# Kernel tuning notes

Measured on AMD Instinct MI355X. Metric: run time of the kernel, lower is better.

## Reference

```python
import jax, jax.numpy as jnp
import numpy as np

K = 5            # kernel_size per dim
KD = K ** 3      # 125 spline weight slots
DIM = 3
NUM_GRAPHS = 64
# (n_nodes, n_edges, c_in, c_mid, c_out) per pyramid level
LEVELS = [(20000, 320000, 1, 32, 64), (10000, 160000, 1, 64, 64),
          (5000, 80000, 1, 64, 64), (2500, 40000, 1, 64, 64), (1250, 20000, 1, 64, 64)]


def setup_inputs() -> dict:
    key = jax.random.key(0)
    inp = {}
    for i, (n, e, cin, c1, c2) in enumerate(LEVELS, start=1):
        ks = jax.random.split(jax.random.fold_in(key, i), 8)
        inp[f'x{i}'] = jax.random.normal(ks[0], (n, cin), jnp.float32)
        inp[f'pseudo{i}'] = jax.random.uniform(ks[1], (e, DIM), jnp.float32)  # in [0,1)
        inp[f'edge_index{i}'] = jax.random.randint(ks[2], (2, e), 0, n)
        inp[f'batch{i}'] = jnp.sort(jax.random.randint(ks[3], (n,), 0, NUM_GRAPHS))
        inp[f'W{i}a'] = 0.1 * jax.random.normal(ks[4], (KD, cin, c1), jnp.float32)
        inp[f'root{i}a'] = 0.1 * jax.random.normal(ks[5], (cin, c1), jnp.float32)
        inp[f'bias{i}a'] = jnp.zeros((c1,), jnp.float32)
        inp[f'W{i}b'] = 0.1 * jax.random.normal(ks[6], (KD, c1, c2), jnp.float32)
        inp[f'root{i}b'] = 0.1 * jax.random.normal(ks[7], (c1, c2), jnp.float32)
        inp[f'bias{i}b'] = jnp.zeros((c2,), jnp.float32)
    kf = jax.random.fold_in(key, 99)
    inp['fc_w'] = 0.05 * jax.random.normal(kf, (5 * 64, 10), jnp.float32)
    inp['fc_b'] = jnp.zeros((10,), jnp.float32)
    return inp


def _spline_conv(x, src, dst, pseudo, W, Wroot, bias):
    """Degree-1 open B-spline conv (torch_spline_conv), mean aggregation + root weight."""
    n, cin = x.shape
    v = pseudo * (K - 1)                       # [E,3], pseudo in [0,1)
    k0 = jnp.floor(v).astype(jnp.int32)        # lower knot index per dim
    frac = v - k0                              # fractional part per dim
    xs = x[src]                                # [E,cin] gather source feats
    # accumulate basis-weighted source features per (target node, kernel slot)
    acc = jnp.zeros((n, KD, cin), x.dtype)
    for bits in range(2 ** DIM):               # 8 corner combinations of linear spline
        w = jnp.ones((src.shape[0],), x.dtype)
        idx = jnp.zeros((src.shape[0],), jnp.int32)
        for d in range(DIM):
            b = (bits >> d) & 1
            w = w * (frac[:, d] if b else 1.0 - frac[:, d])
            idx = idx * K + (k0[:, d] + b)
        acc = acc.at[dst, idx].add(w[:, None] * xs)
    deg = jnp.zeros((n,), x.dtype).at[dst].add(1.0)
    out = jnp.einsum('nki,kio->no', acc, W) / jnp.maximum(deg, 1.0)[:, None]
    return out + x @ Wroot + bias


def _readout(f, batch):
    s = jax.ops.segment_sum(f, batch, num_segments=NUM_GRAPHS)
    cnt = jax.ops.segment_sum(jnp.ones((f.shape[0],), f.dtype), batch, num_segments=NUM_GRAPHS)
    return s / jnp.maximum(cnt, 1.0)[:, None]   # scatter_mean


def _level(x, ei, ps, bt, Wa, ra, ba, Wb, rb, bb):
    f = jax.nn.relu(_spline_conv(x, ei[0], ei[1], ps, Wa, ra, ba))
    f = jax.nn.relu(_spline_conv(f, ei[0], ei[1], ps, Wb, rb, bb))
    return _readout(f, bt)


def reference(x1, pseudo1, edge_index1, batch1, W1a, root1a, bias1a, W1b, root1b, bias1b,
              x2, pseudo2, edge_index2, batch2, W2a, root2a, bias2a, W2b, root2b, bias2b,
              x3, pseudo3, edge_index3, batch3, W3a, root3a, bias3a, W3b, root3b, bias3b,
              x4, pseudo4, edge_index4, batch4, W4a, root4a, bias4a, W4b, root4b, bias4b,
              x5, pseudo5, edge_index5, batch5, W5a, root5a, bias5a, W5b, root5b, bias5b,
              fc_w, fc_b):
    levels = [
        (x1, edge_index1, pseudo1, batch1, W1a, root1a, bias1a, W1b, root1b, bias1b),
        (x2, edge_index2, pseudo2, batch2, W2a, root2a, bias2a, W2b, root2b, bias2b),
        (x3, edge_index3, pseudo3, batch3, W3a, root3a, bias3a, W3b, root3b, bias3b),
        (x4, edge_index4, pseudo4, batch4, W4a, root4a, bias4a, W4b, root4b, bias4b),
        (x5, edge_index5, pseudo5, batch5, W5a, root5a, bias5a, W5b, root5b, bias5b),
    ]
    res = [_level(*lv) for lv in levels]
    h = jnp.concatenate(res, axis=1)            # [B,320]; eval mode -> dropout is identity
    logits = h @ fc_w + fc_b                    # [B,10]
    return jax.nn.log_softmax(logits, axis=1)
```

## Files before the change

### kernel.cpp

```cpp
#include <hip/hip_runtime.h>
#include <hip/hip_fp16.h>
#include <math.h>

#define NUM_GRAPHS 64

typedef unsigned short ushortT;
typedef __attribute__((ext_vector_type(8))) short bf16x8;
typedef __attribute__((ext_vector_type(4))) float f32x4;

constexpr int cN[5]       = {20000, 10000, 5000, 2500, 1250};
constexpr int cE[5]       = {320000, 160000, 80000, 40000, 20000};
constexpr int cNOFF[6]    = {0, 20000, 30000, 35000, 37500, 38750};
constexpr int cEOFF[6]    = {0, 320000, 480000, 560000, 600000, 620000};
constexpr int cEBLKOFF[6] = {0, 1250, 1875, 2188, 2345, 2424};
constexpr int cNBLKOFF[6] = {0, 79, 119, 139, 149, 154};
constexpr int cMT[5]      = {5064, 2564, 1314, 689, 377};
constexpr int cTILEOFF[6] = {0, 5064, 7628, 8942, 9631, 10008};
constexpr int cSEOFF[6]   = {0, 324096, 488192, 572288, 616384, 640512};
constexpr int cF1OFF[6]   = {0, 640000, 1280000, 1600000, 1760000, 1840000};
constexpr int cWOFF[6]    = {0, 32000, 96000, 160000, 224000, 288000};
constexpr int cABLK32[6]  = {0, 625, 938, 1095, 1174, 1214};
constexpr int cRBOFF[5]   = {0, 256, 768, 1280, 1792};
constexpr int cWAOFF[6]   = {0, 512, 1536, 2560, 3584, 4608};
constexpr int cRGB[6]     = {0, 313, 470, 549, 589, 609};
constexpr int cPAIR[6]    = {0, 2532, 3814, 4471, 4816, 5005};

struct P5f { const float* p[5]; };
struct P5i { const int* p[5]; };

__device__ __forceinline__ int lvl_e(int b) {
    return (b >= cEBLKOFF[4]) ? 4 : (b >= cEBLKOFF[3]) ? 3 : (b >= cEBLKOFF[2]) ? 2 : (b >= cEBLKOFF[1]) ? 1 : 0;
}
__device__ __forceinline__ int lvl_n(int b) {
    return (b >= cNBLKOFF[4]) ? 4 : (b >= cNBLKOFF[3]) ? 3 : (b >= cNBLKOFF[2]) ? 2 : (b >= cNBLKOFF[1]) ? 1 : 0;
}

__device__ __forceinline__ ushortT f2bf(float f) {
    union { float f; unsigned int u; } v; v.f = f;
    unsigned int r = (v.u + 0x7FFFu + ((v.u >> 16) & 1u)) >> 16;
    return (ushortT)r;
}
__device__ __forceinline__ float h2f_lo(unsigned int u) {
    return __half2float(__ushort_as_half((ushortT)(u & 0xFFFFu)));
}
__device__ __forceinline__ float h2f_hi(unsigned int u) {
    return __half2float(__ushort_as_half((ushortT)(u >> 16)));
}

__global__ void k_hist(P5f PS, P5i EI, int* __restrict__ dcnt, int* __restrict__ bb) {
    int b = blockIdx.x;
    int l = lvl_e(b);
    int lb = b - cEBLKOFF[l];
    int E = cE[l];
    __shared__ int h[64];
    int t = threadIdx.x;
    if (t < 64) h[t] = 0;
    __syncthreads();
    int e = lb * 256 + t;
    if (e < E) {
        atomicAdd(&dcnt[cNOFF[l] + EI.p[l][E + e]], 1);
        const float* ps = PS.p[l];
        int c = (int)floorf(ps[e * 3] * 4.f) * 16 + (int)floorf(ps[e * 3 + 1] * 4.f) * 4
              + (int)floorf(ps[e * 3 + 2] * 4.f);
        atomicAdd(&h[c], 1);
    }
    __syncthreads();
    if (t < 64) bb[(size_t)b * 64 + t] = h[t];
}

__global__ void k_cellscan(int* __restrict__ bb_all, int* __restrict__ csPad,
                           int* __restrict__ cellTot, int* __restrict__ cot_all) {
    int l = blockIdx.x;
    int c = threadIdx.x;
    int* bb = bb_all + (size_t)cEBLKOFF[l] * 64;
    int nblk = cEBLKOFF[l + 1] - cEBLKOFF[l];
    int run = 0;
    int b = 0;
    for (; b + 16 <= nblk; b += 16) {
        int v[16];
#pragma unroll
        for (int u = 0; u < 16; u++) v[u] = bb[(b + u) * 64 + c];
#pragma unroll
        for (int u = 0; u < 16; u++) { bb[(b + u) * 64 + c] = run; run += v[u]; }
    }
    for (; b < nblk; b++) { int v = bb[b * 64 + c]; bb[b * 64 + c] = run; run += v; }
    int tot = run;
    cellTot[l * 64 + c] = tot;
    int tiles = (tot + 63) >> 6;
    int x = tiles;
#pragma unroll
    for (int off = 1; off < 64; off <<= 1) { int y = __shfl_up(x, off, 64); if (c >= off) x += y; }
    int tileBase = x - tiles;
    csPad[l * 64 + c] = tileBase * 64;
    int* cot = cot_all + cTILEOFF[l];
    for (int i = 0; i < tiles; i++) {
        int vv = tot - (i << 6); if (vv > 64) vv = 64;
        cot[tileBase + i] = c | (vv << 8);
    }
    int nT = __shfl(x, 63, 64);
    int mt = cMT[l];
    for (int i = nT + c; i < mt; i += 64) cot[i] = -1;
}

__global__ void k_nscan1(const int* __restrict__ dcnt, int* __restrict__ dbase, int* __restrict__ bsum) {
    int b = blockIdx.x;
    int l = lvl_n(b);
    int lb = b - cNBLKOFF[l];
    int n = cN[l];
    __shared__ int sh[256];
    int t = threadIdx.x;
    int i = lb * 256 + t;
    int v = (i < n) ? dcnt[cNOFF[l] + i] : 0;
    sh[t] = v;
    __syncthreads();
    for (int off = 1; off < 256; off <<= 1) {
        int y = (t >= off) ? sh[t - off] : 0;
        __syncthreads();
        sh[t] += y;
        __syncthreads();
    }
    if (i < n) dbase[cNOFF[l] + i] = sh[t] - v;
    if (t == 255) bsum[b] = sh[255];
}

__global__ void k_nscan2(const int* __restrict__ bsum, int* __restrict__ boff) {
    int l = blockIdx.x;
    int o = cNBLKOFF[l];
    int nb = cNBLKOFF[l + 1] - o;
    int t = threadIdx.x;
    int v = (t < nb) ? bsum[o + t] : 0;
    int s = v;
#pragma unroll
    for (int off = 1; off < 64; off <<= 1) { int y = __shfl_up(s, off, 64); if (t >= off) s += y; }
    int tot = __shfl(s, 63, 64);
    if (t < nb) boff[o + t] = s - v;
    int t2 = t + 64;
    int v2 = (t2 < nb) ? bsum[o + t2] : 0;
    int s2 = v2;
#pragma unroll
    for (int off = 1; off < 64; off <<= 1) { int y = __shfl_up(s2, off, 64); if (t >= off) s2 += y; }
    if (t2 < nb) boff[o + t2] = tot + s2 - v2;
}

__global__ void k_scatter(P5f PS, P5i EI, const int* __restrict__ bb, const int* __restrict__ csPad,
                          const int* __restrict__ dbase, const int* __restrict__ boff,
                          int* __restrict__ rank,
                          int4* __restrict__ cbrec, int4* __restrict__ darec,
                          int* __restrict__ cpos) {
    int b = blockIdx.x;
    int l = lvl_e(b);
    int lb = b - cEBLKOFF[l];
    int E = cE[l];
    __shared__ int base[64];
    __shared__ int cnt[64];
    int t = threadIdx.x;
    if (t < 64) { base[t] = bb[(size_t)b * 64 + t] + csPad[l * 64 + t]; cnt[t] = 0; }
    __syncthreads();
    int e = lb * 256 + t;
    if (e >= E) return;
    const float* ps = PS.p[l];
    float v0 = ps[e * 3] * 4.f, v1 = ps[e * 3 + 1] * 4.f, v2 = ps[e * 3 + 2] * 4.f;
    float f0 = floorf(v0), f1v = floorf(v1), f2v = floorf(v2);
    int c = (int)f0 * 16 + (int)f1v * 4 + (int)f2v;
    int r = atomicAdd(&cnt[c], 1);
    int posc = base[c] + r;
    const int* ei = EI.p[l];
    int src = ei[e];
    int dst = ei[E + e];
    int posd = dbase[cNOFF[l] + dst] + boff[cNBLKOFF[l] + (dst >> 8)]
             + atomicAdd(&rank[cNOFF[l] + dst], 1);
    unsigned int fxfy = (unsigned int)__half_as_ushort(__float2half(v0 - f0))
                      | ((unsigned int)__half_as_ushort(__float2half(v1 - f1v)) << 16);
    unsigned int fzp  = (unsigned int)__half_as_ushort(__float2half(v2 - f2v));
    int4 rc;
    rc.x = src; rc.y = 0; rc.z = (int)fxfy; rc.w = (int)fzp;
    cbrec[cSEOFF[l] + posc] = rc;
    int4 rd;
    rd.x = src | (dst << 16); rd.y = c; rd.z = (int)fxfy; rd.w = (int)fzp;
    darec[cEOFF[l] + posd] = rd;
    cpos[cEOFF[l] + posd] = posc;
}

__global__ void k_wswz(P5f WB, P5f RootB, P5f WA,
                       uint4* __restrict__ hi4, uint4* __restrict__ rb, uint4* __restrict__ wa) {
    int idx = blockIdx.x * 256 + threadIdx.x;
    if (idx >= 294912) return;
    if (idx < 288000) {
        int l = (idx >= 224000) ? 4 : (idx >= 160000) ? 3 : (idx >= 96000) ? 2 : (idx >= 32000) ? 1 : 0;
        int local = idx - cWOFF[l];
        int T = l ? 2 : 1, C = l ? 64 : 32;
        int lane = local & 63;
        int blk = (local >> 6) & 3;
        int rest = local >> 8;
        int st = rest % T, s = rest / T;
        int q = lane >> 4, n = blk * 16 + (lane & 15);
        const float* W = WB.p[l];
        union { ushortT u[8]; uint4 v; } ph;
#pragma unroll
        for (int j = 0; j < 8; j++) {
            int k = st * 32 + q * 8 + j;
            ph.u[j] = f2bf(W[((size_t)s * C + k) * 64 + n]);
        }
        hi4[idx] = ph.v;
    } else if (idx < 290304) {
        int id2 = idx - 288000;
        int l = (id2 >= 1792) ? 4 : (id2 >= 1280) ? 3 : (id2 >= 768) ? 2 : (id2 >= 256) ? 1 : 0;
        int local = id2 - cRBOFF[l];
        int lane = local & 63;
        int w = (local >> 6) & 3;
        int st = local >> 8;
        int q = lane >> 4, n = w * 16 + (lane & 15);
        const float* R = RootB.p[l];
        union { ushortT u[8]; uint4 v; } ph;
#pragma unroll
        for (int j = 0; j < 8; j++) {
            int k = st * 32 + q * 8 + j;
            ph.u[j] = f2bf(R[k * 64 + n]);
        }
        rb[id2] = ph.v;
    } else {
        int id3 = idx - 290304;
        int l = (id3 >= cWAOFF[4]) ? 4 : (id3 >= cWAOFF[3]) ? 3 : (id3 >= cWAOFF[2]) ? 2 : (id3 >= cWAOFF[1]) ? 1 : 0;
        int local = id3 - cWAOFF[l];
        int C1 = l ? 64 : 32;
        int numN = C1 / 16;
        int lane = local & 63;
        int rest = local >> 6;
        int nb = rest % numN, st = rest / numN;
        int q = lane >> 4, n = nb * 16 + (lane & 15);
        const float* Wsrc = WA.p[l];
        union { ushortT u[8]; uint4 v; } ph;
#pragma unroll
        for (int j = 0; j < 8; j++) {
            int k = st * 32 + q * 8 + j;
            ph.u[j] = (k < 125) ? f2bf(Wsrc[k * C1 + n]) : (ushortT)0;
        }
        wa[id3] = ph.v;
    }
}

__launch_bounds__(256)
__global__ void conv_a_fused(P5f X, P5f RootA, P5f BiasA,
                             const int4* __restrict__ darec, const uint4* __restrict__ wasw,
                             const int* __restrict__ dbase, const int* __restrict__ boff,
                             const int* __restrict__ dcnt, ushortT* __restrict__ f1bf) {
    __shared__ float S[32 * 126];
    __shared__ int infoS[256];
    __shared__ unsigned int fxyS[256];
    __shared__ unsigned int fzS[256];
    __shared__ float xsS[256];
    int b = blockIdx.x;
    int l = (b >= cABLK32[4]) ? 4 : (b >= cABLK32[3]) ? 3 : (b >= cABLK32[2]) ? 2 : (b >= cABLK32[1]) ? 1 : 0;
    int node0 = (b - cABLK32[l]) * 32;
    int n = cN[l];
    int nn = n - node0; if (nn > 32) nn = 32;
    int t = threadIdx.x;
    int lane = t & 63, wv = t >> 6;
    int C1 = l ? 64 : 32;
    int numN = C1 >> 4;
    int nTask = 2 * numN;
    const uint4* wl = wasw + cWAOFF[l];
    uint4 wfrag0[4], wfrag1[4];
    {
        int w0 = wv % numN;
#pragma unroll
        for (int st = 0; st < 4; st++) wfrag0[st] = wl[(st * numN + w0) * 64 + lane];
        if (nTask == 8) {
            int w1 = wv;
#pragma unroll
            for (int st = 0; st < 4; st++) wfrag1[st] = wl[(st * numN + w1) * 64 + lane];
        }
    }
    for (int i = t; i < 32 * 126; i += 256) S[i] = 0.f;
    const int* db = dbase + cNOFF[l];
    const int* bo = boff + cNBLKOFF[l];
    int estart = db[node0] + bo[node0 >> 8];
    int vend = node0 + nn;
    int eend = (vend >= n) ? cE[l] : (db[vend] + bo[vend >> 8]);
    const float* x = X.p[l];
    const int4* dr = darec + cEOFF[l];
    const int bx = t & 1, by = (t >> 1) & 1, bz = (t >> 2) & 1;
    int4 rcur; float xcur;
    if (estart + t < eend) { rcur = dr[estart + t]; xcur = x[rcur.x & 0xFFFF]; }
    for (int cs = estart; cs < eend; cs += 256) {
        if (cs + t < eend) {
            infoS[t] = ((((unsigned int)rcur.x) >> 16) - node0) * 64 + rcur.y;
            fxyS[t] = (unsigned int)rcur.z;
            fzS[t] = (unsigned int)rcur.w;
            xsS[t] = xcur;
        }
        __syncthreads();
        int pn = cs + 256 + t;
        if (pn < eend) { rcur = dr[pn]; xcur = x[rcur.x & 0xFFFF]; }
        int ne = eend - cs; if (ne > 256) ne = 256;
        for (int j = (t >> 3); j < ne; j += 32) {
            int info = infoS[j];
            int nl = info >> 6, cell = info & 63;
            unsigned int uz = fxyS[j];
            float fx = h2f_lo(uz), fy = h2f_hi(uz), fz = h2f_lo(fzS[j]);
            float xs = xsS[j];
            int cx = cell >> 4, cy = (cell >> 2) & 3, cz = cell & 3;
            int slot = (cx + bx) * 25 + (cy + by) * 5 + (cz + bz);
            float wc = (bx ? fx : 1.f - fx) * (by ? fy : 1.f - fy) * (bz ? fz : 1.f - fz);
            atomicAdd(&S[nl * 126 + slot], wc * xs);
        }
        __syncthreads();
    }
    ushortT* Sbf = (ushortT*)S;
    float v[17];
#pragma unroll
    for (int j = 0; j < 17; j++) {
        int i = t + 256 * j;
        int node = i / 136, k = i % 136;
        v[j] = (i < 4352 && k < 126) ? S[node * 126 + k] : 0.f;
    }
    __syncthreads();
#pragma unroll
    for (int j = 0; j < 17; j++) {
        int i = t + 256 * j;
        if (i < 4352) Sbf[i] = f2bf(v[j]);
    }
    __syncthreads();
    int q = lane >> 4, m = lane & 15;
    const int* dcl = dcnt + cNOFF[l];
    ushortT* f1bfl = f1bf + cF1OFF[l];
    auto do_task = [&](int task, const uint4* wf) {
        int g = task / numN;
        int w = task - g * numN;
        f32x4 acc = (f32x4){0.f, 0.f, 0.f, 0.f};
#pragma unroll
        for (int st = 0; st < 4; st++) {
            bf16x8 a = *(const bf16x8*)&Sbf[(16 * g + m) * 136 + st * 32 + q * 8];
            bf16x8 bw = __builtin_bit_cast(bf16x8, wf[st]);
            acc = __builtin_amdgcn_mfma_f32_16x16x32_bf16(a, bw, acc, 0, 0, 0);
        }
        int ch = w * 16 + m;
        float rv = RootA.p[l][ch], bv = BiasA.p[l][ch];
#pragma unroll
        for (int rr = 0; rr < 4; rr++) {
            int row = 16 * g + q * 4 + rr;
            if (row < nn) {
                int gnode = node0 + row;
                int dv = dcl[gnode];
                float d = (float)(dv > 1 ? dv : 1);
                float o = acc[rr] / d + x[gnode] * rv + bv;
                f1bfl[(size_t)gnode * C1 + ch] = f2bf(fmaxf(o, 0.f));
            }
        }
    };
    do_task(wv, wfrag0);
    if (nTask == 8) do_task(wv + 4, wfrag1);
}

__launch_bounds__(256)
__global__ void k_rgemm(const ushortT* __restrict__ f1bf, const uint4* __restrict__ rb,
                        float* __restrict__ f2) {
    int b = blockIdx.x;
    int l = (b >= cRGB[4]) ? 4 : (b >= cRGB[3]) ? 3 : (b >= cRGB[2]) ? 2 : (b >= cRGB[1]) ? 1 : 0;
    int node0 = (b - cRGB[l]) * 64;
    int n = cN[l];
    int nn = n - node0; if (nn > 64) nn = 64;
    int t = threadIdx.x;
    int lane = t & 63, w = t >> 6;
    int q = lane >> 4, m = lane & 15;
    const int CIN = l ? 64 : 32;
    const int T = l ? 2 : 1;
    const ushortT* fl = f1bf + cF1OFF[l];
    const uint4* rbl = rb + cRBOFF[l];
    f32x4 C[4];
#pragma unroll
    for (int mt = 0; mt < 4; mt++) C[mt] = (f32x4){0.f, 0.f, 0.f, 0.f};
    for (int st = 0; st < T; st++) {
        bf16x8 bh = __builtin_bit_cast(bf16x8, rbl[(st * 4 + w) * 64 + lane]);
#pragma unroll
        for (int mt = 0; mt < 4; mt++) {
            int row = 16 * mt + m;
            int nr = node0 + row; if (nr > n - 1) nr = n - 1;
            bf16x8 a = *(const bf16x8*)&fl[(size_t)nr * CIN + st * 32 + q * 8];
            C[mt] = __builtin_amdgcn_mfma_f32_16x16x32_bf16(a, bh, C[mt], 0, 0, 0);
        }
    }
#pragma unroll
    for (int mt = 0; mt < 4; mt++)
#pragma unroll
        for (int rr = 0; rr < 4; rr++) {
            int row = 16 * mt + q * 4 + rr;
            if (row < nn)
                f2[(size_t)(cNOFF[l] + node0 + row) * 64 + 16 * w + m] = C[mt][rr];
        }
}

template<int CIN>
__device__ __forceinline__ void stage_issue(const ushortT* __restrict__ f1bfl, int srcx,
                                            ushortT* lregion, int lane) {
    const int NC = CIN / 8;
#pragma unroll
    for (int i = 0; i < NC; i++) {
        int s = i * 64 + lane;
        int row = s / NC;
        int cp = s & (NC - 1);
        int chunk = cp ^ (row & (NC - 1));
        int src = __shfl(srcx, row, 64);
        const ushortT* gp = f1bfl + (size_t)src * CIN + chunk * 8;
        __builtin_amdgcn_global_load_lds(
            (const __attribute__((address_space(1))) void*)gp,
            (__attribute__((address_space(3))) void*)(lregion + (size_t)i * 512),
            16, 0, 0);
    }
}

template<int CIN>
__device__ __forceinline__ void read_ahr(const ushortT* st, bf16x8 (&ahr)[4][CIN / 32],
                                         int q, int m) {
    const int NC = CIN / 8;
#pragma unroll
    for (int mt = 0; mt < 4; mt++) {
        int row = 16 * mt + m;
#pragma unroll
        for (int s = 0; s < CIN / 32; s++) {
            int chunk = s * 4 + q;
            int cp = chunk ^ (row & (NC - 1));
            ahr[mt][s] = *(const bf16x8*)&st[(size_t)row * NC * 8 + cp * 8];
        }
    }
}

template<int CIN>
__device__ __forceinline__ void conv_b_tile_compute(
    const uint4* __restrict__ whiL, __half* __restrict__ pout,
    bf16x8 (&ahr)[4][CIN / 32], const float* __restrict__ wxy,
    const float* __restrict__ fzp, int cell, int tb, int lane, int wv) {
    const int T = CIN / 32;
    int q = lane >> 4, m = lane & 15;
    int cx = cell >> 4, cy = (cell >> 2) & 3, cz = cell & 3;
    float fzr[16];
#pragma unroll
    for (int mt = 0; mt < 4; mt++)
#pragma unroll
        for (int rr = 0; rr < 4; rr++)
            fzr[mt * 4 + rr] = fzp[16 * mt + q * 4 + rr];

    uint4 wb[2][2 * T];
    auto loadw = [&](int xy, uint4* dst) {
        int bx = xy & 1, by = xy >> 1;
        int s0 = (cx + bx) * 25 + (cy + by) * 5 + cz;
#pragma unroll
        for (int st = 0; st < T; st++) {
            dst[st]     = whiL[((size_t)(s0 * T + st) * 4 + wv) * 64 + lane];
            dst[T + st] = whiL[((size_t)((s0 + 1) * T + st) * 4 + wv) * 64 + lane];
        }
    };
    loadw(0, wb[0]);

    f32x4 acc[4];
#pragma unroll
    for (int mt = 0; mt < 4; mt++) acc[mt] = (f32x4){0.f, 0.f, 0.f, 0.f};

#pragma unroll
    for (int xy = 0; xy < 4; xy++) {
        uint4* cur = wb[xy & 1];
        if (xy < 3) loadw(xy + 1, wb[(xy + 1) & 1]);
        f32x4 C0[4], C1[4];
#pragma unroll
        for (int mt = 0; mt < 4; mt++) {
            C0[mt] = (f32x4){0.f, 0.f, 0.f, 0.f};
            C1[mt] = (f32x4){0.f, 0.f, 0.f, 0.f};
        }
#pragma unroll
        for (int st = 0; st < T; st++) {
            bf16x8 b0 = __builtin_bit_cast(bf16x8, cur[st]);
            bf16x8 b1 = __builtin_bit_cast(bf16x8, cur[T + st]);
#pragma unroll
            for (int mt = 0; mt < 4; mt++) {
                C0[mt] = __builtin_amdgcn_mfma_f32_16x16x32_bf16(ahr[mt][st], b0, C0[mt], 0, 0, 0);
                C1[mt] = __builtin_amdgcn_mfma_f32_16x16x32_bf16(ahr[mt][st], b1, C1[mt], 0, 0, 0);
            }
        }
        const float* wrow = &wxy[xy * 64];
#pragma unroll
        for (int mt = 0; mt < 4; mt++)
#pragma unroll
            for (int rr = 0; rr < 4; rr++) {
                float wxyv = wrow[16 * mt + q * 4 + rr];
                float dlt = C1[mt][rr] - C0[mt][rr];
                float tt = fmaf(fzr[mt * 4 + rr], dlt, C0[mt][rr]);
                acc[mt][rr] = fmaf(wxyv, tt, acc[mt][rr]);
            }
    }
#pragma unroll
    for (int mt = 0; mt < 4; mt++)
#pragma unroll
        for (int rr = 0; rr < 4; rr++) {
            int row = 16 * mt + q * 4 + rr;
            pout[(size_t)(tb + row) * 64 + 16 * wv + m] = __float2half(acc[mt][rr]);
        }
}

template<int CIN>
__device__ __forceinline__ void conv_b_pair(
    const ushortT* __restrict__ f1bfl, const int4* __restrict__ cbl,
    const uint4* __restrict__ whiL, __half* __restrict__ pout,
    int d0, int d1, int tb0, int tb1, int lane, int wv,
    ushortT* stage0, ushortT* stage1,
    float* __restrict__ wxy0, float* __restrict__ fz0,
    float* __restrict__ wxy1, float* __restrict__ fz1) {
    const int T = CIN / 32;
    const int NC = CIN / 8;
    int q = lane >> 4, m = lane & 15;
    bool has1 = d1 >= 0;
    int cell0 = d0 & 63, v0 = d0 >> 8;
    int cell1 = has1 ? (d1 & 63) : 0, v1 = has1 ? (d1 >> 8) : 0;

    int4 r0, r1;
    if (lane < v0) r0 = cbl[tb0 + lane]; else { r0.x = 0; r0.y = 0; r0.z = 0; r0.w = 0; }
    if (lane < v1) r1 = cbl[tb1 + lane]; else { r1.x = 0; r1.y = 0; r1.z = 0; r1.w = 0; }

    {
        unsigned int uz = (unsigned int)r0.z;
        float fx = h2f_lo(uz), fy = h2f_hi(uz);
        float gx = 1.f - fx, gy = 1.f - fy;
        wxy0[0 * 64 + lane] = gx * gy;
        wxy0[1 * 64 + lane] = fx * gy;
        wxy0[2 * 64 + lane] = gx * fy;
        wxy0[3 * 64 + lane] = fx * fy;
        fz0[lane] = h2f_lo((unsigned int)r0.w);
    }
    {
        unsigned int uz = (unsigned int)r1.z;
        float fx = h2f_lo(uz), fy = h2f_hi(uz);
        float gx = 1.f - fx, gy = 1.f - fy;
        wxy1[0 * 64 + lane] = gx * gy;
        wxy1[1 * 64 + lane] = fx * gy;
        wxy1[2 * 64 + lane] = gx * fy;
        wxy1[3 * 64 + lane] = fx * fy;
        fz1[lane] = h2f_lo((unsigned int)r1.w);
    }
    __builtin_amdgcn_wave_barrier();

    stage_issue<CIN>(f1bfl, r0.x, stage0, lane);
    if (has1) stage_issue<CIN>(f1bfl, r1.x, stage1, lane);

    if (has1) {
        if (CIN == 64) asm volatile("s_waitcnt vmcnt(8)" ::: "memory");
        else           asm volatile("s_waitcnt vmcnt(4)" ::: "memory");
    } else {
        asm volatile("s_waitcnt vmcnt(0)" ::: "memory");
    }

    bf16x8 ahr[4][T];
    read_ahr<CIN>(stage0, ahr, q, m);
    conv_b_tile_compute<CIN>(whiL, pout, ahr, wxy0, fz0, cell0, tb0, lane, wv);

    if (has1) {
        asm volatile("s_waitcnt vmcnt(0)" ::: "memory");
        read_ahr<CIN>(stage1, ahr, q, m);
        conv_b_tile_compute<CIN>(whiL, pout, ahr, wxy1, fz1, cell1, tb1, lane, wv);
    }
    (void)NC;
}

__launch_bounds__(256, 2)
__global__ void conv_b_all(const ushortT* __restrict__ f1bf, const int4* __restrict__ cbrec,
                           const uint4* __restrict__ whi, const int* __restrict__ cot,
                           __half* __restrict__ Ph) {
    __shared__ __align__(16) ushortT stageS[2][4096];
    __shared__ float wxyS[2][256];
    __shared__ float fzS[2][64];
    int t = threadIdx.x;
    int wv = t >> 6, lane = t & 63;
    int b = blockIdx.x;
    int l = (b >= cPAIR[4]) ? 4 : (b >= cPAIR[3]) ? 3 : (b >= cPAIR[2]) ? 2 : (b >= cPAIR[1]) ? 1 : 0;
    int p = b - cPAIR[l];
    int t0 = 2 * p, t1 = t0 + 1;
    const int* cotl = cot + cTILEOFF[l];
    int d0 = cotl[t0];
    int d1 = (t1 < cMT[l]) ? cotl[t1] : -1;
    if (d0 < 0) return;
    int tb0 = t0 * 64, tb1 = t1 * 64;
    if (l == 0)
        conv_b_pair<32>(f1bf, cbrec, whi, Ph, d0, d1, tb0, tb1, lane, wv,
                        stageS[0], stageS[1], wxyS[0], fzS[0], wxyS[1], fzS[1]);
    else
        conv_b_pair<64>(f1bf + cF1OFF[l], cbrec + cSEOFF[l], whi + cWOFF[l],
                        Ph + (size_t)cSEOFF[l] * 64, d0, d1, tb0, tb1, lane, wv,
                        stageS[0], stageS[1], wxyS[0], fzS[0], wxyS[1], fzS[1]);
}

__launch_bounds__(256)
__global__ void node_b_all(const __half* __restrict__ Ph, const int* __restrict__ cpos,
                           const int* __restrict__ dbase, const int* __restrict__ boff,
                           const int* __restrict__ dcnt, P5f BiasB, float* __restrict__ f2) {
    int lane = threadIdx.x & 63;
    int blk = blockIdx.x;
    int l, node;
    if (blk < 5000) {
        l = 0;
        node = blk * 4 + (threadIdx.x >> 6);
        if (node >= 20000) return;
    } else {
        const int NB2[4] = {0, 2500, 3750, 4375};
        int b2 = blk - 5000;
        int li = (b2 >= 4375) ? 3 : (b2 >= 3750) ? 2 : (b2 >= 2500) ? 1 : 0;
        l = li + 1;
        node = (b2 - NB2[li]) * 4 + (threadIdx.x >> 6);
        if (node >= cN[l]) return;
    }
    int start = dbase[cNOFF[l] + node] + boff[cNBLKOFF[l] + (node >> 8)];
    int deg = dcnt[cNOFF[l] + node];
    const __half* PhL = Ph + (size_t)cSEOFF[l] * 64;
    const int* cposL = cpos + cEOFF[l];
    float* f2row = f2 + (size_t)(cNOFF[l] + node) * 64;
    float s0 = 0.f, s1 = 0.f, s2 = 0.f, s3 = 0.f;
    int k = 0;
    for (; k + 4 <= deg; k += 4) {
        int r0 = cposL[start + k];
        int r1 = cposL[start + k + 1];
        int r2 = cposL[start + k + 2];
        int r3 = cposL[start + k + 3];
        s0 += __half2float(PhL[(size_t)r0 * 64 + lane]);
        s1 += __half2float(PhL[(size_t)r1 * 64 + lane]);
        s2 += __half2float(PhL[(size_t)r2 * 64 + lane]);
        s3 += __half2float(PhL[(size_t)r3 * 64 + lane]);
    }
    for (; k < deg; k++) s0 += __half2float(PhL[(size_t)cposL[start + k] * 64 + lane]);
    float s = (s0 + s1) + (s2 + s3);
    s /= (float)(deg > 1 ? deg : 1);
    s += f2row[lane] + BiasB.p[l][lane];
    f2row[lane] = fmaxf(s, 0.f);
}

__launch_bounds__(256)
__global__ void k_read(const float* __restrict__ f2, P5i Batch,
                       float* __restrict__ hsum, float* __restrict__ gcnt) {
    const int RC[5] = {0, 1250, 1875, 2188, 2345};
    int t = threadIdx.x;
    int lane = t & 63;
    int w = blockIdx.x * 4 + (t >> 6);
    if (w >= 2424) return;
    int l = (w >= 2345) ? 4 : (w >= 2188) ? 3 : (w >= 1875) ? 2 : (w >= 1250) ? 1 : 0;
    int base = (w - RC[l]) * 16;
    int Nl = cN[l];
    int nn = Nl - base; if (nn > 16) nn = 16;
    const int* batch = Batch.p[l];
    const float* fb = f2 + (size_t)(cNOFF[l] + base) * 64;
    int curg = -1; float hacc = 0.f; int crun = 0;
    for (int j = 0; j < nn; j++) {
        int g = batch[base + j];
        if (g != curg) {
            if (curg >= 0) {
                atomicAdd(&hsum[curg * 320 + l * 64 + lane], hacc);
                if (lane == 0) atomicAdd(&gcnt[l * 64 + curg], (float)crun);
            }
            curg = g; hacc = 0.f; crun = 0;
        }
        hacc += fb[(size_t)j * 64 + lane];
        crun++;
    }
    if (curg >= 0) {
        atomicAdd(&hsum[curg * 320 + l * 64 + lane], hacc);
        if (lane == 0) atomicAdd(&gcnt[l * 64 + curg], (float)crun);
    }
}

__global__ void fc_kernel(const float* __restrict__ hsum, const float* __restrict__ gcnt,
                          const float* __restrict__ fcw, const float* __restrict__ fcb,
                          float* __restrict__ out) {
    int g = blockIdx.x;
    int lane = threadIdx.x;
    float partial[10];
#pragma unroll
    for (int t = 0; t < 10; t++) partial[t] = 0.f;
#pragma unroll
    for (int k = 0; k < 5; k++) {
        int j = k * 64 + lane;
        float c = fmaxf(gcnt[k * 64 + g], 1.f);
        float h = hsum[g * 320 + j] / c;
        const float* fw = fcw + j * 10;
#pragma unroll
        for (int t = 0; t < 10; t++) partial[t] = fmaf(h, fw[t], partial[t]);
    }
#pragma unroll
    for (int off = 32; off >= 1; off >>= 1)
#pragma unroll
        for (int t = 0; t < 10; t++) partial[t] += __shfl_xor(partial[t], off, 64);
    if (lane == 0) {
        float logit[10];
#pragma unroll
        for (int t = 0; t < 10; t++) logit[t] = partial[t] + fcb[t];
        float m = logit[0];
#pragma unroll
        for (int t = 1; t < 10; t++) m = fmaxf(m, logit[t]);
        float sum = 0.f;
#pragma unroll
        for (int t = 0; t < 10; t++) sum += expf(logit[t] - m);
        float lse = m + logf(sum);
#pragma unroll
        for (int t = 0; t < 10; t++) out[g * 10 + t] = logit[t] - lse;
    }
}

extern "C" void kernel_launch(void* const* d_in, const int* in_sizes, int n_in,
                              void* d_out, int out_size, void* d_ws, size_t ws_size,
                              hipStream_t stream) {
    int* wsI = (int*)d_ws;
    int*   dcnt  = wsI;
    int*   rank  = dcnt + 38750;
    float* hsum  = (float*)(rank + 38750);
    float* gcnt  = hsum + 20480;
    float* f2    = gcnt + 320;
    int*   dbase = (int*)(f2 + 2480000);
    int*   bsum  = dbase + 38750;
    int*   boff  = bsum + 160;
    int*   cpos  = boff + 160;
    int*   bb    = cpos + 620000;
    int*   csPad = bb + 155136;
    int*   cellTot = csPad + 320;
    int*   cot   = cellTot + 320;
    int4*  cbrec = (int4*)(((size_t)(cot + 10008) + 15) & ~(size_t)15);
    int4*  darec = cbrec + 640512;
    ushortT* f1bf = (ushortT*)(darec + 620000);
    uint4* whi   = (uint4*)(((size_t)(f1bf + 1840000) + 15) & ~(size_t)15);
    uint4* rbsw  = whi + 288000;
    uint4* wasw  = rbsw + 2304;
    __half* Ph   = (__half*)(wasw + 4608);

    hipMemsetAsync(dcnt, 0, (size_t)(38750 * 2 + 20480 + 320) * sizeof(int), stream);

    P5f PS, X, WA, RootA, BiasA, WB, RootB, BiasB;
    P5i EI, Batch;
    for (int l = 0; l < 5; l++) {
        const int b = l * 10;
        X.p[l]     = (const float*)d_in[b + 0];
        PS.p[l]    = (const float*)d_in[b + 1];
        EI.p[l]    = (const int*)d_in[b + 2];
        Batch.p[l] = (const int*)d_in[b + 3];
        WA.p[l]    = (const float*)d_in[b + 4];
        RootA.p[l] = (const float*)d_in[b + 5];
        BiasA.p[l] = (const float*)d_in[b + 6];
        WB.p[l]    = (const float*)d_in[b + 7];
        RootB.p[l] = (const float*)d_in[b + 8];
        BiasB.p[l] = (const float*)d_in[b + 9];
    }

    k_hist<<<2424, 256, 0, stream>>>(PS, EI, dcnt, bb);
    k_cellscan<<<5, 64, 0, stream>>>(bb, csPad, cellTot, cot);
    k_nscan1<<<154, 256, 0, stream>>>(dcnt, dbase, bsum);
    k_nscan2<<<5, 64, 0, stream>>>(bsum, boff);
    k_scatter<<<2424, 256, 0, stream>>>(PS, EI, bb, csPad, dbase, boff, rank,
                                        cbrec, darec, cpos);
    k_wswz<<<1152, 256, 0, stream>>>(WB, RootB, WA, whi, rbsw, wasw);

    conv_a_fused<<<1214, 256, 0, stream>>>(X, RootA, BiasA, darec, wasw,
                                           dbase, boff, dcnt, f1bf);

    k_rgemm<<<609, 256, 0, stream>>>(f1bf, rbsw, f2);

    conv_b_all<<<5005, 256, 0, stream>>>(f1bf, cbrec, whi, cot, Ph);
    node_b_all<<<9688, 256, 0, stream>>>(Ph, cpos, dbase, boff, dcnt, BiasB, f2);

    k_read<<<606, 256, 0, stream>>>(f2, Batch, hsum, gcnt);
    fc_kernel<<<64, 64, 0, stream>>>(hsum, gcnt, (const float*)d_in[50], (const float*)d_in[51],
                                     (float*)d_out);
}
```

Before: 433.3 us.

## Scatter conv outputs to destination order and parallelize per-cell scan across waves

The conv_b kernel now writes each edge's half-precision message directly to its destination-sorted slot, using a per-edge position stored in the cell-sorted record. The node reduction can then read contiguous rows instead of going through the cpos indirection array, and the cpos array is no longer written. Separately, the serial per-cell block scan, which ran on only 5 blocks, is split into a wave-parallel shuffle scan over 80 blocks plus a small tile-assignment kernel. In exchange, conv_b's output stores become scattered rather than contiguous, and there is one extra kernel launch.

```diff
diff --git a/kernel.cpp b/kernel.cpp
--- a/kernel.cpp
+++ b/kernel.cpp
@@ -68,24 +68,30 @@
     if (t < 64) bb[(size_t)b * 64 + t] = h[t];
 }
 
-__global__ void k_cellscan(int* __restrict__ bb_all, int* __restrict__ csPad,
-                           int* __restrict__ cellTot, int* __restrict__ cot_all) {
-    int l = blockIdx.x;
-    int c = threadIdx.x;
+__global__ void k_cellscan1(int* __restrict__ bb_all, int* __restrict__ cellTot) {
+    int W = blockIdx.x * 4 + (threadIdx.x >> 6);
+    int lane = threadIdx.x & 63;
+    int l = W >> 6, c = W & 63;
     int* bb = bb_all + (size_t)cEBLKOFF[l] * 64;
     int nblk = cEBLKOFF[l + 1] - cEBLKOFF[l];
     int run = 0;
-    int b = 0;
-    for (; b + 16 <= nblk; b += 16) {
-        int v[16];
-#pragma unroll
-        for (int u = 0; u < 16; u++) v[u] = bb[(b + u) * 64 + c];
-#pragma unroll
-        for (int u = 0; u < 16; u++) { bb[(b + u) * 64 + c] = run; run += v[u]; }
-    }
-    for (; b < nblk; b++) { int v = bb[b * 64 + c]; bb[b * 64 + c] = run; run += v; }
-    int tot = run;
-    cellTot[l * 64 + c] = tot;
+    for (int b0 = 0; b0 < nblk; b0 += 64) {
+        int b = b0 + lane;
+        int v = (b < nblk) ? bb[b * 64 + c] : 0;
+        int s = v;
+#pragma unroll
+        for (int off = 1; off < 64; off <<= 1) { int y = __shfl_up(s, off, 64); if (lane >= off) s += y; }
+        if (b < nblk) bb[b * 64 + c] = run + s - v;
+        run += __shfl(s, 63, 64);
+    }
+    if (lane == 0) cellTot[l * 64 + c] = run;
+}
+
+__global__ void k_cellscan2(const int* __restrict__ cellTot, int* __restrict__ csPad,
+                            int* __restrict__ cot_all) {
+    int l = blockIdx.x;
+    int c = threadIdx.x;
+    int tot = cellTot[l * 64 + c];
     int tiles = (tot + 63) >> 6;
     int x = tiles;
 #pragma unroll
@@ -145,8 +151,7 @@
 __global__ void k_scatter(P5f PS, P5i EI, const int* __restrict__ bb, const int* __restrict__ csPad,
                           const int* __restrict__ dbase, const int* __restrict__ boff,
                           int* __restrict__ rank,
-                          int4* __restrict__ cbrec, int4* __restrict__ darec,
-                          int* __restrict__ cpos) {
+                          int4* __restrict__ cbrec, int4* __restrict__ darec) {
     int b = blockIdx.x;
     int l = lvl_e(b);
     int lb = b - cEBLKOFF[l];
@@ -173,12 +178,11 @@
                       | ((unsigned int)__half_as_ushort(__float2half(v1 - f1v)) << 16);
     unsigned int fzp  = (unsigned int)__half_as_ushort(__float2half(v2 - f2v));
     int4 rc;
-    rc.x = src; rc.y = 0; rc.z = (int)fxfy; rc.w = (int)fzp;
+    rc.x = src; rc.y = posd; rc.z = (int)fxfy; rc.w = (int)fzp;
     cbrec[cSEOFF[l] + posc] = rc;
     int4 rd;
     rd.x = src | (dst << 16); rd.y = c; rd.z = (int)fxfy; rd.w = (int)fzp;
     darec[cEOFF[l] + posd] = rd;
-    cpos[cEOFF[l] + posd] = posc;
 }
 
 __global__ void k_wswz(P5f WB, P5f RootB, P5f WA,
@@ -429,7 +433,8 @@
 __device__ __forceinline__ void conv_b_tile_compute(
     const uint4* __restrict__ whiL, __half* __restrict__ pout,
     bf16x8 (&ahr)[4][CIN / 32], const float* __restrict__ wxy,
-    const float* __restrict__ fzp, int cell, int tb, int lane, int wv) {
+    const float* __restrict__ fzp, const int* __restrict__ pd, int valid,
+    int cell, int lane, int wv) {
     const int T = CIN / 32;
     int q = lane >> 4, m = lane & 15;
     int cx = cell >> 4, cy = (cell >> 2) & 3, cz = cell & 3;
@@ -492,7 +497,8 @@
 #pragma unroll
         for (int rr = 0; rr < 4; rr++) {
             int row = 16 * mt + q * 4 + rr;
-            pout[(size_t)(tb + row) * 64 + 16 * wv + m] = __float2half(acc[mt][rr]);
+            if (row < valid)
+                pout[(size_t)pd[row] * 64 + 16 * wv + m] = __float2half(acc[mt][rr]);
         }
 }
 
@@ -502,10 +508,9 @@
     const uint4* __restrict__ whiL, __half* __restrict__ pout,
     int d0, int d1, int tb0, int tb1, int lane, int wv,
     ushortT* stage0, ushortT* stage1,
-    float* __restrict__ wxy0, float* __restrict__ fz0,
-    float* __restrict__ wxy1, float* __restrict__ fz1) {
+    float* __restrict__ wxy0, float* __restrict__ fz0, int* __restrict__ pd0,
+    float* __restrict__ wxy1, float* __restrict__ fz1, int* __restrict__ pd1) {
     const int T = CIN / 32;
-    const int NC = CIN / 8;
     int q = lane >> 4, m = lane & 15;
     bool has1 = d1 >= 0;
     int cell0 = d0 & 63, v0 = d0 >> 8;
@@ -524,6 +529,7 @@
         wxy0[2 * 64 + lane] = gx * fy;
         wxy0[3 * 64 + lane] = fx * fy;
         fz0[lane] = h2f_lo((unsigned int)r0.w);
+        pd0[lane] = r0.y;
     }
     {
         unsigned int uz = (unsigned int)r1.z;
@@ -534,6 +540,7 @@
         wxy1[2 * 64 + lane] = gx * fy;
         wxy1[3 * 64 + lane] = fx * fy;
         fz1[lane] = h2f_lo((unsigned int)r1.w);
+        pd1[lane] = r1.y;
     }
     __builtin_amdgcn_wave_barrier();
 
@@ -549,14 +556,13 @@
 
     bf16x8 ahr[4][T];
     read_ahr<CIN>(stage0, ahr, q, m);
-    conv_b_tile_compute<CIN>(whiL, pout, ahr, wxy0, fz0, cell0, tb0, lane, wv);
+    conv_b_tile_compute<CIN>(whiL, pout, ahr, wxy0, fz0, pd0, v0, cell0, lane, wv);
 
     if (has1) {
         asm volatile("s_waitcnt vmcnt(0)" ::: "memory");
         read_ahr<CIN>(stage1, ahr, q, m);
-        conv_b_tile_compute<CIN>(whiL, pout, ahr, wxy1, fz1, cell1, tb1, lane, wv);
-    }
-    (void)NC;
+        conv_b_tile_compute<CIN>(whiL, pout, ahr, wxy1, fz1, pd1, v1, cell1, lane, wv);
+    }
 }
 
 __launch_bounds__(256, 2)
@@ -566,6 +572,7 @@
     __shared__ __align__(16) ushortT stageS[2][4096];
     __shared__ float wxyS[2][256];
     __shared__ float fzS[2][64];
+    __shared__ int pdS[2][64];
     int t = threadIdx.x;
     int wv = t >> 6, lane = t & 63;
     int b = blockIdx.x;
@@ -579,15 +586,17 @@
     int tb0 = t0 * 64, tb1 = t1 * 64;
     if (l == 0)
         conv_b_pair<32>(f1bf, cbrec, whi, Ph, d0, d1, tb0, tb1, lane, wv,
-                        stageS[0], stageS[1], wxyS[0], fzS[0], wxyS[1], fzS[1]);
+                        stageS[0], stageS[1],
+                        wxyS[0], fzS[0], pdS[0], wxyS[1], fzS[1], pdS[1]);
     else
         conv_b_pair<64>(f1bf + cF1OFF[l], cbrec + cSEOFF[l], whi + cWOFF[l],
-                        Ph + (size_t)cSEOFF[l] * 64, d0, d1, tb0, tb1, lane, wv,
-                        stageS[0], stageS[1], wxyS[0], fzS[0], wxyS[1], fzS[1]);
+                        Ph + (size_t)cEOFF[l] * 64, d0, d1, tb0, tb1, lane, wv,
+                        stageS[0], stageS[1],
+                        wxyS[0], fzS[0], pdS[0], wxyS[1], fzS[1], pdS[1]);
 }
 
 __launch_bounds__(256)
-__global__ void node_b_all(const __half* __restrict__ Ph, const int* __restrict__ cpos,
+__global__ void node_b_all(const __half* __restrict__ Ph,
                            const int* __restrict__ dbase, const int* __restrict__ boff,
                            const int* __restrict__ dcnt, P5f BiasB, float* __restrict__ f2) {
     int lane = threadIdx.x & 63;
@@ -607,22 +616,17 @@
     }
     int start = dbase[cNOFF[l] + node] + boff[cNBLKOFF[l] + (node >> 8)];
     int deg = dcnt[cNOFF[l] + node];
-    const __half* PhL = Ph + (size_t)cSEOFF[l] * 64;
-    const int* cposL = cpos + cEOFF[l];
+    const __half* PhL = Ph + (size_t)cEOFF[l] * 64;
     float* f2row = f2 + (size_t)(cNOFF[l] + node) * 64;
     float s0 = 0.f, s1 = 0.f, s2 = 0.f, s3 = 0.f;
     int k = 0;
     for (; k + 4 <= deg; k += 4) {
-        int r0 = cposL[start + k];
-        int r1 = cposL[start + k + 1];
-        int r2 = cposL[start + k + 2];
-        int r3 = cposL[start + k + 3];
-        s0 += __half2float(PhL[(size_t)r0 * 64 + lane]);
-        s1 += __half2float(PhL[(size_t)r1 * 64 + lane]);
-        s2 += __half2float(PhL[(size_t)r2 * 64 + lane]);
-        s3 += __half2float(PhL[(size_t)r3 * 64 + lane]);
-    }
-    for (; k < deg; k++) s0 += __half2float(PhL[(size_t)cposL[start + k] * 64 + lane]);
+        s0 += __half2float(PhL[(size_t)(start + k) * 64 + lane]);
+        s1 += __half2float(PhL[(size_t)(start + k + 1) * 64 + lane]);
+        s2 += __half2float(PhL[(size_t)(start + k + 2) * 64 + lane]);
+        s3 += __half2float(PhL[(size_t)(start + k + 3) * 64 + lane]);
+    }
+    for (; k < deg; k++) s0 += __half2float(PhL[(size_t)(start + k) * 64 + lane]);
     float s = (s0 + s1) + (s2 + s3);
     s /= (float)(deg > 1 ? deg : 1);
     s += f2row[lane] + BiasB.p[l][lane];
@@ -743,11 +747,12 @@
     }
 
     k_hist<<<2424, 256, 0, stream>>>(PS, EI, dcnt, bb);
-    k_cellscan<<<5, 64, 0, stream>>>(bb, csPad, cellTot, cot);
+    k_cellscan1<<<80, 256, 0, stream>>>(bb, cellTot);
+    k_cellscan2<<<5, 64, 0, stream>>>(cellTot, csPad, cot);
     k_nscan1<<<154, 256, 0, stream>>>(dcnt, dbase, bsum);
     k_nscan2<<<5, 64, 0, stream>>>(bsum, boff);
     k_scatter<<<2424, 256, 0, stream>>>(PS, EI, bb, csPad, dbase, boff, rank,
-                                        cbrec, darec, cpos);
+                                        cbrec, darec);
     k_wswz<<<1152, 256, 0, stream>>>(WB, RootB, WA, whi, rbsw, wasw);
 
     conv_a_fused<<<1214, 256, 0, stream>>>(X, RootA, BiasA, darec, wasw,
@@ -756,7 +761,7 @@
     k_rgemm<<<609, 256, 0, stream>>>(f1bf, rbsw, f2);
 
     conv_b_all<<<5005, 256, 0, stream>>>(f1bf, cbrec, whi, cot, Ph);
-    node_b_all<<<9688, 256, 0, stream>>>(Ph, cpos, dbase, boff, dcnt, BiasB, f2);
+    node_b_all<<<9688, 256, 0, stream>>>(Ph, dbase, boff, dcnt, BiasB, f2);
 
     k_read<<<606, 256, 0, stream>>>(f2, Batch, hsum, gcnt);
     fc_kernel<<<64, 64, 0, stream>>>(hsum, gcnt, (const float*)d_in[50], (const float*)d_in[51],
```

New measurement: 427.7 us. About the same (-1.3%).
